# Kernel optimization log

Measured on AMD Instinct MI355X. Metric: run time of the kernel, lower is better.

## Reference

```python
import jax, jax.numpy as jnp
import numpy as np

N_NODES = 50000
N_EDGES = 800000
IN_C = 64
HID = 128
OUT_C = 2
N_GRAPHS = 64


def setup_inputs() -> dict:
    key = jax.random.key(0)
    ks = jax.random.split(key, 12)
    x = jax.random.normal(ks[0], (N_NODES, IN_C), dtype=jnp.float32)
    edge_index = jax.random.randint(ks[1], (2, N_EDGES), 0, N_NODES, dtype=jnp.int64)
    batch = jnp.sort(jax.random.randint(ks[2], (N_NODES,), 0, N_GRAPHS, dtype=jnp.int64))
    def glorot(k, shape):
        lim = float(np.sqrt(6.0 / (shape[0] + shape[1])))
        return jax.random.uniform(k, shape, dtype=jnp.float32, minval=-lim, maxval=lim)
    return {
        "x": x,
        "edge_index": edge_index,
        "batch": batch,
        "W1": glorot(ks[3], (IN_C, HID)),  "b1": jnp.zeros((HID,), jnp.float32),
        "W2": glorot(ks[4], (HID, HID)),   "b2": jnp.zeros((HID,), jnp.float32),
        "Wm1": glorot(ks[5], (HID, HID)),  "bm1": jnp.zeros((HID,), jnp.float32),
        "Wm2": glorot(ks[6], (HID, OUT_C)), "bm2": jnp.zeros((OUT_C,), jnp.float32),
    }


def reference(x, edge_index, batch, W1, b1, W2, b2, Wm1, bm1, Wm2, bm2):
    N = x.shape[0]
    # GCN normalization with self-loops (PyG GCNConv defaults)
    loops = jnp.arange(N, dtype=edge_index.dtype)
    src = jnp.concatenate([edge_index[0], loops])  # message sources
    dst = jnp.concatenate([edge_index[1], loops])  # aggregation targets
    deg = jax.ops.segment_sum(jnp.ones(dst.shape, x.dtype), dst, num_segments=N)
    dinv = jnp.where(deg > 0, jax.lax.rsqrt(deg), 0.0)
    norm = dinv[src] * dinv[dst]  # [E+N]

    def gcn_conv(h, W, b):
        h = h @ W                         # transform first (PyG order)
        msg = h[src] * norm[:, None]      # gather + normalize
        return jax.ops.segment_sum(msg, dst, num_segments=N) + b  # scatter-add

    h = jax.nn.relu(gcn_conv(x, W1, b1))
    # dropout is identity in eval mode
    h = gcn_conv(h, W2, b2)

    # global mean pool over graphs
    sums = jax.ops.segment_sum(h, batch, num_segments=N_GRAPHS)
    cnt = jax.ops.segment_sum(jnp.ones((N,), h.dtype), batch, num_segments=N_GRAPHS)
    g = sums / jnp.maximum(cnt, 1.0)[:, None]  # [G, HID]

    g = jax.nn.relu(g @ Wm1 + bm1)
    return g @ Wm2 + bm2  # [G, OUT_C]
```

## Files before the change

kernel.cpp:

```cpp
#include <hip/hip_runtime.h>
#include <stdint.h>

#define N_NODES 50000
#define N_EDGES 800000
#define IN_C 64
#define HID 128
#define OUT_C 2
#define N_GRAPHS 64
#define NBUCK 196
#define BCAP 6144
#define ECH 4096

typedef long long i64;
typedef __attribute__((ext_vector_type(8))) short bf8;
typedef __attribute__((ext_vector_type(4))) float f32x4;

__device__ __forceinline__ float bf2f(ushort h) {
    return __uint_as_float(((uint)h) << 16);
}
__device__ __forceinline__ ushort f2bf(float f) {
    uint x = __float_as_uint(f);
    uint r = x + 0x7fffu + ((x >> 16) & 1u);
    return (ushort)(r >> 16);
}
__device__ __forceinline__ float loadf(const void* p, size_t i, int bf) {
    return bf ? bf2f(((const ushort*)p)[i]) : ((const float*)p)[i];
}
__device__ __forceinline__ int clampi(int v, int lo, int hi) {
    return min(max(v, lo), hi);
}

__device__ __forceinline__ int edge_src(const void* ei, int e, int wide) {
    return wide ? (int)((const i64*)ei)[e] : ((const int*)ei)[e];
}
__device__ __forceinline__ int edge_dst(const void* ei, int e, int wide) {
    return wide ? (int)((const i64*)ei)[N_EDGES + e] : ((const int*)ei)[N_EDGES + e];
}
__device__ __forceinline__ i64 batch_at(const void* b, int i, int wide) {
    return wide ? ((const i64*)b)[i] : (i64)((const int*)b)[i];
}

__global__ __launch_bounds__(256) void k_init(const uint* __restrict__ braw,
                                              const uint* __restrict__ xraw,
                                              int* __restrict__ bcnt,
                                              float* __restrict__ gbuf,
                                              int* __restrict__ iflag,
                                              int* __restrict__ fflag) {
    int i = blockIdx.x * blockDim.x + threadIdx.x;
    if (i < N_GRAPHS * HID) gbuf[i] = 0.f;
    if (i < NBUCK) bcnt[i] = 0;
    if (blockIdx.x == 0) {
        __shared__ uint si[128];
        __shared__ int sf[256];
        int t = threadIdx.x;
        if (t < 128) si[t] = (t < 100) ? braw[25001 + 2 * t] : 0u;
        uint e = (xraw[t] >> 7) & 0xFFu;
        sf[t] = (e >= 100u && e <= 140u) ? 1 : 0;
        __syncthreads();
        for (int off = 128; off > 0; off >>= 1) {
            if (t < off) {
                sf[t] += sf[t + off];
                if (off <= 64 && t < 64) si[t] |= si[t + off];
            }
            __syncthreads();
        }
        if (t == 0) {
            *iflag = (si[0] == 0u) ? 1 : 0;
            *fflag = (sf[0] >= 192) ? 1 : 0;
        }
    }
}

__global__ __launch_bounds__(1024) void k_binA(const void* __restrict__ ei,
                                               const int* __restrict__ iflag,
                                               const int* __restrict__ fflag,
                                               const void* __restrict__ W1,
                                               const void* __restrict__ W2,
                                               ushort* __restrict__ Wt1,
                                               ushort* __restrict__ Wt2,
                                               int* __restrict__ bcnt,
                                               uint2* __restrict__ bmem) {
    int t = threadIdx.x;
    if (t < 256 && blockIdx.x < (IN_C * HID + HID * HID) / 256) {
        int ff = *fflag;
        int idx = blockIdx.x * 256 + t;
        if (idx < IN_C * HID) {
            int k = idx >> 7, n = idx & 127;
            Wt1[n * IN_C + k] = f2bf(loadf(W1, idx, ff));
        } else {
            int j = idx - IN_C * HID;
            int k = j >> 7, n = j & 127;
            Wt2[n * HID + k] = f2bf(loadf(W2, j, ff));
        }
    }
    int wide = *iflag;
    __shared__ int cnt[NBUCK];
    __shared__ int obase[NBUCK];
    __shared__ int run[NBUCK];
    __shared__ int gbase[NBUCK];
    __shared__ int sc[256];
    __shared__ uint2 stage[ECH];
    int e0 = blockIdx.x * ECH;
    int m = min(ECH, N_EDGES - e0);
    for (int i = t; i < NBUCK; i += 1024) cnt[i] = 0;
    __syncthreads();
    for (int i = t; i < m; i += 1024) {
        int d = edge_dst(ei, e0 + i, wide);
        atomicAdd(&cnt[d >> 8], 1);
    }
    __syncthreads();
    int cv = (t < NBUCK) ? cnt[t] : 0;
    if (t < 256) sc[t] = cv;
    __syncthreads();
    for (int off = 1; off < 256; off <<= 1) {
        int v = (t >= off && t < 256) ? sc[t - off] : 0;
        __syncthreads();
        if (t < 256) sc[t] += v;
        __syncthreads();
    }
    if (t < NBUCK) {
        int ex = sc[t] - cv;
        obase[t] = ex;
        run[t] = ex;
        gbase[t] = (cv > 0) ? atomicAdd(&bcnt[t], cv) : 0;
    }
    __syncthreads();
    for (int i = t; i < m; i += 1024) {
        int s = edge_src(ei, e0 + i, wide);
        int d = edge_dst(ei, e0 + i, wide);
        int slot = atomicAdd(&run[d >> 8], 1);
        uint2 pr;
        pr.x = (uint)s;
        pr.y = (uint)d;
        stage[slot] = pr;
    }
    __syncthreads();
    for (int i = t; i < m; i += 1024) {
        uint2 pr = stage[i];
        int b = (int)(pr.y >> 8);
        int pos = gbase[b] + (i - obase[b]);
        if (pos < BCAP) bmem[(size_t)b * BCAP + pos] = pr;
    }
}

__global__ __launch_bounds__(1024) void k_binB(const uint2* __restrict__ bmem,
                                               const int* __restrict__ bcnt,
                                               const void* __restrict__ x,
                                               const int* __restrict__ fflag,
                                               int* __restrict__ offs,
                                               int* __restrict__ csr,
                                               float* __restrict__ dinv,
                                               ushort* __restrict__ Y1) {
    int b = blockIdx.x;
    int t = threadIdx.x;
    int node0 = b << 8;
    __shared__ int sc[256];
    __shared__ int degl[256];
    __shared__ int run[256];
    __shared__ float sdinv[256];
    __shared__ int sbase, scnt;
    __shared__ int stage[BCAP];
    int v = (t < NBUCK) ? bcnt[t] : 0;
    if (t < 256) sc[t] = v;
    __syncthreads();
    for (int off = 1; off < 256; off <<= 1) {
        int u = (t >= off && t < 256) ? sc[t - off] : 0;
        __syncthreads();
        if (t < 256) sc[t] += u;
        __syncthreads();
    }
    if (t == b) {
        int c = clampi(v, 0, BCAP);
        scnt = c;
        sbase = clampi(sc[t] - v, 0, N_EDGES - c);
    }
    if (t < 256) degl[t] = 0;
    __syncthreads();
    int cnt = scnt;
    int base = sbase;
    for (int i = t; i < cnt; i += 1024) {
        uint2 pr = bmem[(size_t)b * BCAP + i];
        atomicAdd(&degl[pr.y & 255], 1);
    }
    __syncthreads();
    int dv = (t < 256) ? degl[t] : 0;
    if (t < 256) sc[t] = dv;
    __syncthreads();
    for (int off = 1; off < 256; off <<= 1) {
        int u = (t >= off && t < 256) ? sc[t - off] : 0;
        __syncthreads();
        if (t < 256) sc[t] += u;
        __syncthreads();
    }
    if (t < 256) {
        int ex = sc[t] - dv;
        run[t] = ex;
        float di = rsqrtf((float)(dv + 1));
        sdinv[t] = di;
        int n = node0 + t;
        if (n < N_NODES) {
            offs[n] = base + ex;
            dinv[n] = di;
        }
    }
    if (b == 0 && t == 0) offs[N_NODES] = N_EDGES;
    __syncthreads();
    for (int i = t; i < cnt; i += 1024) {
        uint2 pr = bmem[(size_t)b * BCAP + i];
        int slot = atomicAdd(&run[pr.y & 255], 1);
        stage[clampi(slot, 0, BCAP - 1)] = (int)pr.x;
    }
    __syncthreads();
    for (int i = t; i < cnt; i += 1024) csr[base + i] = stage[i];
    int ff = *fflag;
    for (int idx = t; idx < 256 * (IN_C / 4); idx += 1024) {
        int nl = idx >> 4, c4 = (idx & 15) * 4;
        int nn = node0 + nl;
        if (nn < N_NODES) {
            float x0, x1, x2, x3;
            if (ff) {
                const ushort* xp = (const ushort*)x + (size_t)nn * IN_C + c4;
                ushort4 u = *(const ushort4*)xp;
                x0 = bf2f(u.x); x1 = bf2f(u.y); x2 = bf2f(u.z); x3 = bf2f(u.w);
            } else {
                const float* xp = (const float*)x + (size_t)nn * IN_C + c4;
                float4 vv = *(const float4*)xp;
                x0 = vv.x; x1 = vv.y; x2 = vv.z; x3 = vv.w;
            }
            float di = sdinv[nl];
            ushort4 o;
            o.x = f2bf(x0 * di); o.y = f2bf(x1 * di);
            o.z = f2bf(x2 * di); o.w = f2bf(x3 * di);
            *(ushort4*)(Y1 + (size_t)nn * IN_C + c4) = o;
        }
    }
}

__global__ __launch_bounds__(256) void k_aggM(const ushort* __restrict__ Y1,
                                              const float* __restrict__ dinv,
                                              const int* __restrict__ offs,
                                              const int* __restrict__ csr,
                                              ushort* __restrict__ M) {
    int n = (blockIdx.x * blockDim.x + threadIdx.x) >> 4;
    int lane = threadIdx.x & 15;
    if (n >= N_NODES) return;
    const uint* y32 = (const uint*)Y1;
    size_t rb = (size_t)n * 32;
    uint s0 = y32[rb + lane];
    uint s1 = y32[rb + lane + 16];
    float a0 = bf2f((ushort)(s0 & 0xffffu));
    float a1 = bf2f((ushort)(s0 >> 16));
    float a2 = bf2f((ushort)(s1 & 0xffffu));
    float a3 = bf2f((ushort)(s1 >> 16));
    int s = offs[n];
    int e = min(offs[n + 1], s + 4096);
    int i = s;
    for (; i + 8 <= e; i += 8) {
        uint u0[8], u1[8];
#pragma unroll
        for (int k = 0; k < 8; k++) {
            size_t r = (size_t)csr[i + k] * 32;
            u0[k] = y32[r + lane];
            u1[k] = y32[r + lane + 16];
        }
#pragma unroll
        for (int k = 0; k < 8; k++) {
            a0 += bf2f((ushort)(u0[k] & 0xffffu));
            a1 += bf2f((ushort)(u0[k] >> 16));
            a2 += bf2f((ushort)(u1[k] & 0xffffu));
            a3 += bf2f((ushort)(u1[k] >> 16));
        }
    }
    for (; i < e; i++) {
        size_t r = (size_t)csr[i] * 32;
        uint u0 = y32[r + lane];
        uint u1 = y32[r + lane + 16];
        a0 += bf2f((ushort)(u0 & 0xffffu));
        a1 += bf2f((ushort)(u0 >> 16));
        a2 += bf2f((ushort)(u1 & 0xffffu));
        a3 += bf2f((ushort)(u1 >> 16));
    }
    float dv = dinv[n];
    ((uint*)M)[rb + lane] = ((uint)f2bf(a1 * dv) << 16) | (uint)f2bf(a0 * dv);
    ((uint*)M)[rb + lane + 16] = ((uint)f2bf(a3 * dv) << 16) | (uint)f2bf(a2 * dv);
}

__global__ __launch_bounds__(256) void k_agg128(const ushort* __restrict__ hs,
                                                const float* __restrict__ dinv,
                                                const int* __restrict__ offs,
                                                const int* __restrict__ csr,
                                                ushort* __restrict__ out) {
    int n = (blockIdx.x * blockDim.x + threadIdx.x) >> 5;
    int lane = threadIdx.x & 31;
    if (n >= N_NODES) return;
    const uint* hs32 = (const uint*)hs;
    size_t rb = (size_t)n * 64;
    uint s0 = hs32[rb + lane];
    uint s1 = hs32[rb + lane + 32];
    float a0 = bf2f((ushort)(s0 & 0xffffu));
    float a1 = bf2f((ushort)(s0 >> 16));
    float a2 = bf2f((ushort)(s1 & 0xffffu));
    float a3 = bf2f((ushort)(s1 >> 16));
    int s = offs[n];
    int e = min(offs[n + 1], s + 4096);
    int i = s;
    for (; i + 8 <= e; i += 8) {
        uint u0[8], u1[8];
#pragma unroll
        for (int k = 0; k < 8; k++) {
            size_t r = (size_t)csr[i + k] * 64;
            u0[k] = hs32[r + lane];
            u1[k] = hs32[r + lane + 32];
        }
#pragma unroll
        for (int k = 0; k < 8; k++) {
            a0 += bf2f((ushort)(u0[k] & 0xffffu));
            a1 += bf2f((ushort)(u0[k] >> 16));
            a2 += bf2f((ushort)(u1[k] & 0xffffu));
            a3 += bf2f((ushort)(u1[k] >> 16));
        }
    }
    for (; i < e; i++) {
        size_t r = (size_t)csr[i] * 64;
        uint u0 = hs32[r + lane];
        uint u1 = hs32[r + lane + 32];
        a0 += bf2f((ushort)(u0 & 0xffffu));
        a1 += bf2f((ushort)(u0 >> 16));
        a2 += bf2f((ushort)(u1 & 0xffffu));
        a3 += bf2f((ushort)(u1 >> 16));
    }
    float dv = dinv[n];
    ((uint*)out)[rb + lane] = ((uint)f2bf(a1 * dv) << 16) | (uint)f2bf(a0 * dv);
    ((uint*)out)[rb + lane + 32] = ((uint)f2bf(a3 * dv) << 16) | (uint)f2bf(a2 * dv);
}

template <int K>
__global__ __launch_bounds__(256) void k_gemm_f(const ushort* __restrict__ A,
                                                const ushort* __restrict__ Wt,
                                                const int* __restrict__ fflag,
                                                const float* __restrict__ dinv,
                                                const void* __restrict__ bias,
                                                ushort* __restrict__ out) {
    int ff = *fflag;
    int wave = threadIdx.x >> 6;
    int lane = threadIdx.x & 63;
    int m16 = lane & 15;
    int q = lane >> 4;
    int rowbase = blockIdx.x * 64 + wave * 16;
    int arow = min(rowbase + m16, N_NODES - 1);

    f32x4 acc[8];
#pragma unroll
    for (int t = 0; t < 8; t++) acc[t] = (f32x4){0.f, 0.f, 0.f, 0.f};

#pragma unroll
    for (int kc = 0; kc < K; kc += 32) {
        bf8 a = *(const bf8*)(A + (size_t)arow * K + kc + q * 8);
#pragma unroll
        for (int t = 0; t < 8; t++) {
            bf8 b = *(const bf8*)(Wt + (size_t)(t * 16 + m16) * K + kc + q * 8);
            acc[t] = __builtin_amdgcn_mfma_f32_16x16x32_bf16(a, b, acc[t], 0, 0, 0);
        }
    }

    float dv[4];
    int rowok[4];
#pragma unroll
    for (int r = 0; r < 4; r++) {
        int row = rowbase + q * 4 + r;
        rowok[r] = (row < N_NODES);
        dv[r] = rowok[r] ? dinv[row] : 1.f;
    }
#pragma unroll
    for (int t = 0; t < 8; t++) {
        int col = t * 16 + m16;
        float bv = loadf(bias, col, ff);
#pragma unroll
        for (int r = 0; r < 4; r++) {
            int row = rowbase + q * 4 + r;
            if (rowok[r]) {
                float v = fmaxf(acc[t][r] + bv, 0.f) * dv[r];
                out[(size_t)row * HID + col] = f2bf(v);
            }
        }
    }
}

__global__ __launch_bounds__(256) void k_gemm_pool(const ushort* __restrict__ A,
                                                   const ushort* __restrict__ Wt,
                                                   const void* __restrict__ batch,
                                                   const int* __restrict__ iflag,
                                                   float* __restrict__ gsum) {
    const int K = HID;
    int wide = *iflag;
    int tid = threadIdx.x;
    int wave = tid >> 6;
    int lane = tid & 63;
    int m16 = lane & 15;
    int q = lane >> 4;
    int rowbase = blockIdx.x * 64 + wave * 16;
    int arow = min(rowbase + m16, N_NODES - 1);

    __shared__ float sacc[64][HID];
    __shared__ int sbg[64];

    if (tid < 64) {
        int n = blockIdx.x * 64 + tid;
        int g = (n < N_NODES) ? (int)batch_at(batch, n, wide) : -1;
        sbg[tid] = (g < 0 || g >= N_GRAPHS) ? -1 : g;
    }

    f32x4 acc[8];
#pragma unroll
    for (int t = 0; t < 8; t++) acc[t] = (f32x4){0.f, 0.f, 0.f, 0.f};

#pragma unroll
    for (int kc = 0; kc < K; kc += 32) {
        bf8 a = *(const bf8*)(A + (size_t)arow * K + kc + q * 8);
#pragma unroll
        for (int t = 0; t < 8; t++) {
            bf8 b = *(const bf8*)(Wt + (size_t)(t * 16 + m16) * K + kc + q * 8);
            acc[t] = __builtin_amdgcn_mfma_f32_16x16x32_bf16(a, b, acc[t], 0, 0, 0);
        }
    }

#pragma unroll
    for (int t = 0; t < 8; t++) {
        int col = t * 16 + m16;
#pragma unroll
        for (int r = 0; r < 4; r++) {
            int rl = wave * 16 + q * 4 + r;
            int row = rowbase + q * 4 + r;
            sacc[rl][col] = (row < N_NODES) ? acc[t][r] : 0.f;
        }
    }
    __syncthreads();

    int col = tid & 127;
    int half = tid >> 7;
    int gcur = -1;
    float a = 0.f;
    for (int r = half * 32; r < half * 32 + 32; r++) {
        int g = sbg[r];
        if (g != gcur) {
            if (gcur >= 0) atomicAdd(&gsum[gcur * HID + col], a);
            a = 0.f;
            gcur = g;
        }
        a += sacc[r][col];
    }
    if (gcur >= 0) atomicAdd(&gsum[gcur * HID + col], a);
}

__global__ void k_mlp(const float* __restrict__ gsum, const void* __restrict__ batch,
                      const int* __restrict__ iflag, const void* __restrict__ b2,
                      const void* __restrict__ Wm1, const void* __restrict__ bm1,
                      const void* __restrict__ Wm2, const void* __restrict__ bm2,
                      const int* __restrict__ fflag, float* __restrict__ out) {
    int ff = *fflag;
    int wide = *iflag;
    int gr = blockIdx.x;
    int c = threadIdx.x;
    int lo = 0, hi = N_NODES;
    while (lo < hi) { int m = (lo + hi) >> 1; if (batch_at(batch, m, wide) < (i64)gr) lo = m + 1; else hi = m; }
    int s = lo;
    lo = s; hi = N_NODES;
    while (lo < hi) { int m = (lo + hi) >> 1; if (batch_at(batch, m, wide) < (i64)(gr + 1)) lo = m + 1; else hi = m; }
    float cnt = (float)(lo - s);

    __shared__ float sg[HID];
    __shared__ float r0[HID], r1[HID];
    sg[c] = gsum[gr * HID + c] / fmaxf(cnt, 1.0f) + loadf(b2, c, ff);
    __syncthreads();
    float acc = loadf(bm1, c, ff);
#pragma unroll 8
    for (int k = 0; k < HID; k++) acc += sg[k] * loadf(Wm1, k * HID + c, ff);
    float hid = fmaxf(acc, 0.f);
    r0[c] = hid * loadf(Wm2, c * OUT_C + 0, ff);
    r1[c] = hid * loadf(Wm2, c * OUT_C + 1, ff);
    __syncthreads();
    for (int off = 64; off > 0; off >>= 1) {
        if (c < off) { r0[c] += r0[c + off]; r1[c] += r1[c + off]; }
        __syncthreads();
    }
    if (c == 0) {
        out[gr * OUT_C + 0] = r0[0] + loadf(bm2, 0, ff);
        out[gr * OUT_C + 1] = r1[0] + loadf(bm2, 1, ff);
    }
}


extern "C" void kernel_launch(void* const* d_in, const int* in_sizes, int n_in,
                              void* d_out, int out_size, void* d_ws, size_t ws_size,
                              hipStream_t stream) {
    const void* x     = d_in[0];
    const void* ei    = d_in[1];
    const void* batch = d_in[2];
    const void* W1  = d_in[3];
    const void* b1  = d_in[4];
    const void* W2  = d_in[5];
    const void* b2  = d_in[6];
    const void* Wm1 = d_in[7];
    const void* bm1 = d_in[8];
    const void* Wm2 = d_in[9];
    const void* bm2 = d_in[10];

    char* p = (char*)d_ws;
    auto alloc = [&](size_t bytes) {
        char* r = p;
        p += (bytes + 255) & ~(size_t)255;
        return r;
    };
    int*    iflag  = (int*)alloc(4);
    int*    fflag  = (int*)alloc(4);
    int*    bcnt   = (int*)alloc(NBUCK * 4);
    uint2*  bmem   = (uint2*)alloc((size_t)NBUCK * BCAP * 8);
    float*  dinv   = (float*)alloc(N_NODES * 4);
    int*    offs   = (int*)alloc((N_NODES + 1) * 4);
    int*    csr    = (int*)alloc(N_EDGES * 4);
    ushort* Wt1    = (ushort*)alloc(IN_C * HID * 2);
    ushort* Wt2    = (ushort*)alloc(HID * HID * 2);
    ushort* Y1     = (ushort*)alloc((size_t)N_NODES * IN_C * 2);
    ushort* Mbuf   = (ushort*)alloc((size_t)N_NODES * IN_C * 2);
    ushort* h1s    = (ushort*)alloc((size_t)N_NODES * HID * 2);
    ushort* N2     = (ushort*)alloc((size_t)N_NODES * HID * 2);
    float*  gbuf   = (float*)alloc(N_GRAPHS * HID * 4);

    k_init<<<(N_GRAPHS * HID + 255) / 256, 256, 0, stream>>>(
        (const uint*)batch, (const uint*)x, bcnt, gbuf, iflag, fflag);
    k_binA<<<(N_EDGES + ECH - 1) / ECH, 1024, 0, stream>>>(
        ei, iflag, fflag, W1, W2, Wt1, Wt2, bcnt, bmem);
    k_binB<<<NBUCK, 1024, 0, stream>>>(bmem, bcnt, x, fflag, offs, csr, dinv, Y1);

    k_aggM<<<(N_NODES * 16 + 255) / 256, 256, 0, stream>>>(Y1, dinv, offs, csr, Mbuf);
    k_gemm_f<IN_C><<<(N_NODES + 63) / 64, 256, 0, stream>>>(Mbuf, Wt1, fflag, dinv, b1, h1s);
    k_agg128<<<(N_NODES * 32 + 255) / 256, 256, 0, stream>>>(h1s, dinv, offs, csr, N2);
    k_gemm_pool<<<(N_NODES + 63) / 64, 256, 0, stream>>>(N2, Wt2, batch, iflag, gbuf);

    k_mlp<<<N_GRAPHS, HID, 0, stream>>>(gbuf, batch, iflag, b2, Wm1, bm1, Wm2, bm2, fflag, (float*)d_out);
}
```

Baseline: 204.2 us.

## Fuse all pipeline stages into one persistent kernel with grid barriers

Replaces the sequence of binning, aggregation, GEMM, pooling and MLP kernels with one persistent 256-block kernel. The stages are separated by atomic-counter grid barriers, and each stage runs as a grid-stride loop over the same blocks. This removes launch overhead and inter-kernel gaps, but it depends on all 256 blocks of 1024 threads being co-resident. The shared-memory union and the split-K MFMA with shared atomics in the pool stage may also lower occupancy and per-stage efficiency, and the spin barrier has a timeout fallback that could break correctness.

```diff
diff --git a/kernel.cpp b/kernel.cpp
--- a/kernel.cpp
+++ b/kernel.cpp
@@ -9,7 +9,11 @@
 #define N_GRAPHS 64
 #define NBUCK 196
 #define BCAP 6144
-#define ECH 4096
+#define MECH 3125
+#define MCHUNK 256
+#define NTILE 782
+#define GRID 256
+#define TPB 1024
 
 typedef long long i64;
 typedef __attribute__((ext_vector_type(8))) short bf8;
@@ -40,15 +44,33 @@
     return wide ? ((const i64*)b)[i] : (i64)((const int*)b)[i];
 }
 
-__global__ __launch_bounds__(256) void k_init(const uint* __restrict__ braw,
+__device__ __forceinline__ void gbar(int* __restrict__ bars, int idx) {
+    __syncthreads();
+    if (threadIdx.x == 0) {
+        __threadfence();
+        __hip_atomic_fetch_add(&bars[idx], 1, __ATOMIC_ACQ_REL,
+                               __HIP_MEMORY_SCOPE_AGENT);
+        long long spin = 0;
+        while (__hip_atomic_load(&bars[idx], __ATOMIC_ACQUIRE,
+                                 __HIP_MEMORY_SCOPE_AGENT) < GRID) {
+            __builtin_amdgcn_s_sleep(8);
+            if (++spin > 2000000) break;
+        }
+    }
+    __syncthreads();
+}
+
+__global__ __launch_bounds__(256) void k_prep(const uint* __restrict__ braw,
                                               const uint* __restrict__ xraw,
+                                              int* __restrict__ bars,
                                               int* __restrict__ bcnt,
                                               float* __restrict__ gbuf,
                                               int* __restrict__ iflag,
                                               int* __restrict__ fflag) {
     int i = blockIdx.x * blockDim.x + threadIdx.x;
+    if (i < 16) bars[i] = 0;
+    if (i < NBUCK) bcnt[i] = 0;
     if (i < N_GRAPHS * HID) gbuf[i] = 0.f;
-    if (i < NBUCK) bcnt[i] = 0;
     if (blockIdx.x == 0) {
         __shared__ uint si[128];
         __shared__ int sf[256];
@@ -71,421 +93,414 @@
     }
 }
 
-__global__ __launch_bounds__(1024) void k_binA(const void* __restrict__ ei,
-                                               const int* __restrict__ iflag,
-                                               const int* __restrict__ fflag,
-                                               const void* __restrict__ W1,
-                                               const void* __restrict__ W2,
-                                               ushort* __restrict__ Wt1,
-                                               ushort* __restrict__ Wt2,
-                                               int* __restrict__ bcnt,
-                                               uint2* __restrict__ bmem) {
-    int t = threadIdx.x;
-    if (t < 256 && blockIdx.x < (IN_C * HID + HID * HID) / 256) {
+
+struct SmA {
+    int cnt[NBUCK]; int obase[NBUCK]; int run[NBUCK]; int gbase[NBUCK];
+    int sc[256]; uint2 stage[MECH];
+};
+struct SmB {
+    int sc[256]; int degl[256]; int run[256]; float sdinv[256];
+    int sbase, scnt; int stage[BCAP];
+};
+struct SmP {
+    float sacc[64][HID]; int sbg[64];
+};
+struct SmM {
+    float sg[8][HID]; float r0[8][HID]; float r1[8][HID];
+};
+union MegaSm { SmA a; SmB b; SmP p; SmM m; };
+
+__global__ __launch_bounds__(TPB) void k_mega(
+    const void* __restrict__ x, const void* __restrict__ ei,
+    const void* __restrict__ batch,
+    const void* __restrict__ W1, const void* __restrict__ b1,
+    const void* __restrict__ W2, const void* __restrict__ b2,
+    const void* __restrict__ Wm1, const void* __restrict__ bm1,
+    const void* __restrict__ Wm2, const void* __restrict__ bm2,
+    int* __restrict__ bars, int* __restrict__ bcnt, uint2* __restrict__ bmem,
+    float* __restrict__ dinv, int* __restrict__ offs, int* __restrict__ csr,
+    ushort* __restrict__ Wt1, ushort* __restrict__ Wt2,
+    ushort* __restrict__ Y1, ushort* __restrict__ Mbuf,
+    ushort* __restrict__ h1s, ushort* __restrict__ N2,
+    float* __restrict__ gbuf, const int* __restrict__ iflag,
+    const int* __restrict__ fflag, float* __restrict__ outp) {
+    __shared__ MegaSm sm;
+    int tid = threadIdx.x;
+    int gsz = gridDim.x;
+
+    {
         int ff = *fflag;
-        int idx = blockIdx.x * 256 + t;
-        if (idx < IN_C * HID) {
-            int k = idx >> 7, n = idx & 127;
-            Wt1[n * IN_C + k] = f2bf(loadf(W1, idx, ff));
-        } else {
-            int j = idx - IN_C * HID;
-            int k = j >> 7, n = j & 127;
-            Wt2[n * HID + k] = f2bf(loadf(W2, j, ff));
-        }
-    }
-    int wide = *iflag;
-    __shared__ int cnt[NBUCK];
-    __shared__ int obase[NBUCK];
-    __shared__ int run[NBUCK];
-    __shared__ int gbase[NBUCK];
-    __shared__ int sc[256];
-    __shared__ uint2 stage[ECH];
-    int e0 = blockIdx.x * ECH;
-    int m = min(ECH, N_EDGES - e0);
-    for (int i = t; i < NBUCK; i += 1024) cnt[i] = 0;
-    __syncthreads();
-    for (int i = t; i < m; i += 1024) {
-        int d = edge_dst(ei, e0 + i, wide);
-        atomicAdd(&cnt[d >> 8], 1);
-    }
-    __syncthreads();
-    int cv = (t < NBUCK) ? cnt[t] : 0;
-    if (t < 256) sc[t] = cv;
-    __syncthreads();
-    for (int off = 1; off < 256; off <<= 1) {
-        int v = (t >= off && t < 256) ? sc[t - off] : 0;
-        __syncthreads();
-        if (t < 256) sc[t] += v;
-        __syncthreads();
-    }
-    if (t < NBUCK) {
-        int ex = sc[t] - cv;
-        obase[t] = ex;
-        run[t] = ex;
-        gbase[t] = (cv > 0) ? atomicAdd(&bcnt[t], cv) : 0;
-    }
-    __syncthreads();
-    for (int i = t; i < m; i += 1024) {
-        int s = edge_src(ei, e0 + i, wide);
-        int d = edge_dst(ei, e0 + i, wide);
-        int slot = atomicAdd(&run[d >> 8], 1);
-        uint2 pr;
-        pr.x = (uint)s;
-        pr.y = (uint)d;
-        stage[slot] = pr;
-    }
-    __syncthreads();
-    for (int i = t; i < m; i += 1024) {
-        uint2 pr = stage[i];
-        int b = (int)(pr.y >> 8);
-        int pos = gbase[b] + (i - obase[b]);
-        if (pos < BCAP) bmem[(size_t)b * BCAP + pos] = pr;
-    }
-}
-
-__global__ __launch_bounds__(1024) void k_binB(const uint2* __restrict__ bmem,
-                                               const int* __restrict__ bcnt,
-                                               const void* __restrict__ x,
-                                               const int* __restrict__ fflag,
-                                               int* __restrict__ offs,
-                                               int* __restrict__ csr,
-                                               float* __restrict__ dinv,
-                                               ushort* __restrict__ Y1) {
-    int b = blockIdx.x;
-    int t = threadIdx.x;
-    int node0 = b << 8;
-    __shared__ int sc[256];
-    __shared__ int degl[256];
-    __shared__ int run[256];
-    __shared__ float sdinv[256];
-    __shared__ int sbase, scnt;
-    __shared__ int stage[BCAP];
-    int v = (t < NBUCK) ? bcnt[t] : 0;
-    if (t < 256) sc[t] = v;
-    __syncthreads();
-    for (int off = 1; off < 256; off <<= 1) {
-        int u = (t >= off && t < 256) ? sc[t - off] : 0;
-        __syncthreads();
-        if (t < 256) sc[t] += u;
-        __syncthreads();
-    }
-    if (t == b) {
-        int c = clampi(v, 0, BCAP);
-        scnt = c;
-        sbase = clampi(sc[t] - v, 0, N_EDGES - c);
-    }
-    if (t < 256) degl[t] = 0;
-    __syncthreads();
-    int cnt = scnt;
-    int base = sbase;
-    for (int i = t; i < cnt; i += 1024) {
-        uint2 pr = bmem[(size_t)b * BCAP + i];
-        atomicAdd(&degl[pr.y & 255], 1);
-    }
-    __syncthreads();
-    int dv = (t < 256) ? degl[t] : 0;
-    if (t < 256) sc[t] = dv;
-    __syncthreads();
-    for (int off = 1; off < 256; off <<= 1) {
-        int u = (t >= off && t < 256) ? sc[t - off] : 0;
-        __syncthreads();
-        if (t < 256) sc[t] += u;
-        __syncthreads();
-    }
-    if (t < 256) {
-        int ex = sc[t] - dv;
-        run[t] = ex;
-        float di = rsqrtf((float)(dv + 1));
-        sdinv[t] = di;
-        int n = node0 + t;
-        if (n < N_NODES) {
-            offs[n] = base + ex;
-            dinv[n] = di;
-        }
-    }
-    if (b == 0 && t == 0) offs[N_NODES] = N_EDGES;
-    __syncthreads();
-    for (int i = t; i < cnt; i += 1024) {
-        uint2 pr = bmem[(size_t)b * BCAP + i];
-        int slot = atomicAdd(&run[pr.y & 255], 1);
-        stage[clampi(slot, 0, BCAP - 1)] = (int)pr.x;
-    }
-    __syncthreads();
-    for (int i = t; i < cnt; i += 1024) csr[base + i] = stage[i];
-    int ff = *fflag;
-    for (int idx = t; idx < 256 * (IN_C / 4); idx += 1024) {
-        int nl = idx >> 4, c4 = (idx & 15) * 4;
-        int nn = node0 + nl;
-        if (nn < N_NODES) {
-            float x0, x1, x2, x3;
-            if (ff) {
-                const ushort* xp = (const ushort*)x + (size_t)nn * IN_C + c4;
-                ushort4 u = *(const ushort4*)xp;
-                x0 = bf2f(u.x); x1 = bf2f(u.y); x2 = bf2f(u.z); x3 = bf2f(u.w);
-            } else {
-                const float* xp = (const float*)x + (size_t)nn * IN_C + c4;
-                float4 vv = *(const float4*)xp;
-                x0 = vv.x; x1 = vv.y; x2 = vv.z; x3 = vv.w;
-            }
-            float di = sdinv[nl];
-            ushort4 o;
-            o.x = f2bf(x0 * di); o.y = f2bf(x1 * di);
-            o.z = f2bf(x2 * di); o.w = f2bf(x3 * di);
-            *(ushort4*)(Y1 + (size_t)nn * IN_C + c4) = o;
-        }
-    }
-}
-
-__global__ __launch_bounds__(256) void k_aggM(const ushort* __restrict__ Y1,
-                                              const float* __restrict__ dinv,
-                                              const int* __restrict__ offs,
-                                              const int* __restrict__ csr,
-                                              ushort* __restrict__ M) {
-    int n = (blockIdx.x * blockDim.x + threadIdx.x) >> 4;
-    int lane = threadIdx.x & 15;
-    if (n >= N_NODES) return;
-    const uint* y32 = (const uint*)Y1;
-    size_t rb = (size_t)n * 32;
-    uint s0 = y32[rb + lane];
-    uint s1 = y32[rb + lane + 16];
-    float a0 = bf2f((ushort)(s0 & 0xffffu));
-    float a1 = bf2f((ushort)(s0 >> 16));
-    float a2 = bf2f((ushort)(s1 & 0xffffu));
-    float a3 = bf2f((ushort)(s1 >> 16));
-    int s = offs[n];
-    int e = min(offs[n + 1], s + 4096);
-    int i = s;
-    for (; i + 8 <= e; i += 8) {
-        uint u0[8], u1[8];
-#pragma unroll
-        for (int k = 0; k < 8; k++) {
-            size_t r = (size_t)csr[i + k] * 32;
-            u0[k] = y32[r + lane];
-            u1[k] = y32[r + lane + 16];
-        }
-#pragma unroll
-        for (int k = 0; k < 8; k++) {
-            a0 += bf2f((ushort)(u0[k] & 0xffffu));
-            a1 += bf2f((ushort)(u0[k] >> 16));
-            a2 += bf2f((ushort)(u1[k] & 0xffffu));
-            a3 += bf2f((ushort)(u1[k] >> 16));
-        }
-    }
-    for (; i < e; i++) {
-        size_t r = (size_t)csr[i] * 32;
-        uint u0 = y32[r + lane];
-        uint u1 = y32[r + lane + 16];
-        a0 += bf2f((ushort)(u0 & 0xffffu));
-        a1 += bf2f((ushort)(u0 >> 16));
-        a2 += bf2f((ushort)(u1 & 0xffffu));
-        a3 += bf2f((ushort)(u1 >> 16));
-    }
-    float dv = dinv[n];
-    ((uint*)M)[rb + lane] = ((uint)f2bf(a1 * dv) << 16) | (uint)f2bf(a0 * dv);
-    ((uint*)M)[rb + lane + 16] = ((uint)f2bf(a3 * dv) << 16) | (uint)f2bf(a2 * dv);
-}
-
-__global__ __launch_bounds__(256) void k_agg128(const ushort* __restrict__ hs,
-                                                const float* __restrict__ dinv,
-                                                const int* __restrict__ offs,
-                                                const int* __restrict__ csr,
-                                                ushort* __restrict__ out) {
-    int n = (blockIdx.x * blockDim.x + threadIdx.x) >> 5;
-    int lane = threadIdx.x & 31;
-    if (n >= N_NODES) return;
-    const uint* hs32 = (const uint*)hs;
-    size_t rb = (size_t)n * 64;
-    uint s0 = hs32[rb + lane];
-    uint s1 = hs32[rb + lane + 32];
-    float a0 = bf2f((ushort)(s0 & 0xffffu));
-    float a1 = bf2f((ushort)(s0 >> 16));
-    float a2 = bf2f((ushort)(s1 & 0xffffu));
-    float a3 = bf2f((ushort)(s1 >> 16));
-    int s = offs[n];
-    int e = min(offs[n + 1], s + 4096);
-    int i = s;
-    for (; i + 8 <= e; i += 8) {
-        uint u0[8], u1[8];
-#pragma unroll
-        for (int k = 0; k < 8; k++) {
-            size_t r = (size_t)csr[i + k] * 64;
-            u0[k] = hs32[r + lane];
-            u1[k] = hs32[r + lane + 32];
-        }
-#pragma unroll
-        for (int k = 0; k < 8; k++) {
-            a0 += bf2f((ushort)(u0[k] & 0xffffu));
-            a1 += bf2f((ushort)(u0[k] >> 16));
-            a2 += bf2f((ushort)(u1[k] & 0xffffu));
-            a3 += bf2f((ushort)(u1[k] >> 16));
-        }
-    }
-    for (; i < e; i++) {
-        size_t r = (size_t)csr[i] * 64;
-        uint u0 = hs32[r + lane];
-        uint u1 = hs32[r + lane + 32];
-        a0 += bf2f((ushort)(u0 & 0xffffu));
-        a1 += bf2f((ushort)(u0 >> 16));
-        a2 += bf2f((ushort)(u1 & 0xffffu));
-        a3 += bf2f((ushort)(u1 >> 16));
-    }
-    float dv = dinv[n];
-    ((uint*)out)[rb + lane] = ((uint)f2bf(a1 * dv) << 16) | (uint)f2bf(a0 * dv);
-    ((uint*)out)[rb + lane + 32] = ((uint)f2bf(a3 * dv) << 16) | (uint)f2bf(a2 * dv);
-}
-
-template <int K>
-__global__ __launch_bounds__(256) void k_gemm_f(const ushort* __restrict__ A,
-                                                const ushort* __restrict__ Wt,
-                                                const int* __restrict__ fflag,
-                                                const float* __restrict__ dinv,
-                                                const void* __restrict__ bias,
-                                                ushort* __restrict__ out) {
-    int ff = *fflag;
-    int wave = threadIdx.x >> 6;
-    int lane = threadIdx.x & 63;
-    int m16 = lane & 15;
-    int q = lane >> 4;
-    int rowbase = blockIdx.x * 64 + wave * 16;
-    int arow = min(rowbase + m16, N_NODES - 1);
-
-    f32x4 acc[8];
-#pragma unroll
-    for (int t = 0; t < 8; t++) acc[t] = (f32x4){0.f, 0.f, 0.f, 0.f};
-
-#pragma unroll
-    for (int kc = 0; kc < K; kc += 32) {
-        bf8 a = *(const bf8*)(A + (size_t)arow * K + kc + q * 8);
-#pragma unroll
-        for (int t = 0; t < 8; t++) {
-            bf8 b = *(const bf8*)(Wt + (size_t)(t * 16 + m16) * K + kc + q * 8);
-            acc[t] = __builtin_amdgcn_mfma_f32_16x16x32_bf16(a, b, acc[t], 0, 0, 0);
-        }
-    }
-
-    float dv[4];
-    int rowok[4];
-#pragma unroll
-    for (int r = 0; r < 4; r++) {
-        int row = rowbase + q * 4 + r;
-        rowok[r] = (row < N_NODES);
-        dv[r] = rowok[r] ? dinv[row] : 1.f;
-    }
-#pragma unroll
-    for (int t = 0; t < 8; t++) {
-        int col = t * 16 + m16;
-        float bv = loadf(bias, col, ff);
-#pragma unroll
-        for (int r = 0; r < 4; r++) {
-            int row = rowbase + q * 4 + r;
-            if (rowok[r]) {
-                float v = fmaxf(acc[t][r] + bv, 0.f) * dv[r];
-                out[(size_t)row * HID + col] = f2bf(v);
-            }
-        }
-    }
-}
-
-__global__ __launch_bounds__(256) void k_gemm_pool(const ushort* __restrict__ A,
-                                                   const ushort* __restrict__ Wt,
-                                                   const void* __restrict__ batch,
-                                                   const int* __restrict__ iflag,
-                                                   float* __restrict__ gsum) {
-    const int K = HID;
-    int wide = *iflag;
-    int tid = threadIdx.x;
-    int wave = tid >> 6;
-    int lane = tid & 63;
-    int m16 = lane & 15;
-    int q = lane >> 4;
-    int rowbase = blockIdx.x * 64 + wave * 16;
-    int arow = min(rowbase + m16, N_NODES - 1);
-
-    __shared__ float sacc[64][HID];
-    __shared__ int sbg[64];
-
-    if (tid < 64) {
-        int n = blockIdx.x * 64 + tid;
-        int g = (n < N_NODES) ? (int)batch_at(batch, n, wide) : -1;
-        sbg[tid] = (g < 0 || g >= N_GRAPHS) ? -1 : g;
-    }
-
-    f32x4 acc[8];
-#pragma unroll
-    for (int t = 0; t < 8; t++) acc[t] = (f32x4){0.f, 0.f, 0.f, 0.f};
-
-#pragma unroll
-    for (int kc = 0; kc < K; kc += 32) {
-        bf8 a = *(const bf8*)(A + (size_t)arow * K + kc + q * 8);
-#pragma unroll
-        for (int t = 0; t < 8; t++) {
-            bf8 b = *(const bf8*)(Wt + (size_t)(t * 16 + m16) * K + kc + q * 8);
-            acc[t] = __builtin_amdgcn_mfma_f32_16x16x32_bf16(a, b, acc[t], 0, 0, 0);
-        }
-    }
-
-#pragma unroll
-    for (int t = 0; t < 8; t++) {
-        int col = t * 16 + m16;
-#pragma unroll
-        for (int r = 0; r < 4; r++) {
-            int rl = wave * 16 + q * 4 + r;
-            int row = rowbase + q * 4 + r;
-            sacc[rl][col] = (row < N_NODES) ? acc[t][r] : 0.f;
-        }
-    }
-    __syncthreads();
-
-    int col = tid & 127;
-    int half = tid >> 7;
-    int gcur = -1;
-    float a = 0.f;
-    for (int r = half * 32; r < half * 32 + 32; r++) {
-        int g = sbg[r];
-        if (g != gcur) {
-            if (gcur >= 0) atomicAdd(&gsum[gcur * HID + col], a);
-            a = 0.f;
-            gcur = g;
-        }
-        a += sacc[r][col];
-    }
-    if (gcur >= 0) atomicAdd(&gsum[gcur * HID + col], a);
-}
-
-__global__ void k_mlp(const float* __restrict__ gsum, const void* __restrict__ batch,
-                      const int* __restrict__ iflag, const void* __restrict__ b2,
-                      const void* __restrict__ Wm1, const void* __restrict__ bm1,
-                      const void* __restrict__ Wm2, const void* __restrict__ bm2,
-                      const int* __restrict__ fflag, float* __restrict__ out) {
-    int ff = *fflag;
-    int wide = *iflag;
-    int gr = blockIdx.x;
-    int c = threadIdx.x;
-    int lo = 0, hi = N_NODES;
-    while (lo < hi) { int m = (lo + hi) >> 1; if (batch_at(batch, m, wide) < (i64)gr) lo = m + 1; else hi = m; }
-    int s = lo;
-    lo = s; hi = N_NODES;
-    while (lo < hi) { int m = (lo + hi) >> 1; if (batch_at(batch, m, wide) < (i64)(gr + 1)) lo = m + 1; else hi = m; }
-    float cnt = (float)(lo - s);
-
-    __shared__ float sg[HID];
-    __shared__ float r0[HID], r1[HID];
-    sg[c] = gsum[gr * HID + c] / fmaxf(cnt, 1.0f) + loadf(b2, c, ff);
-    __syncthreads();
-    float acc = loadf(bm1, c, ff);
+        for (int w = blockIdx.x; w < 24; w += gsz) {
+            int idx = w * 1024 + tid;
+            if (idx < IN_C * HID) {
+                int k = idx >> 7, n = idx & 127;
+                Wt1[n * IN_C + k] = f2bf(loadf(W1, idx, ff));
+            } else if (idx < IN_C * HID + HID * HID) {
+                int j = idx - IN_C * HID;
+                int k = j >> 7, n = j & 127;
+                Wt2[n * HID + k] = f2bf(loadf(W2, j, ff));
+            }
+        }
+        int wide = *iflag;
+        for (int ch = blockIdx.x; ch < MCHUNK; ch += gsz) {
+            int e0 = ch * MECH;
+            __syncthreads();
+            for (int i = tid; i < NBUCK; i += TPB) sm.a.cnt[i] = 0;
+            __syncthreads();
+            for (int i = tid; i < MECH; i += TPB) {
+                int d = edge_dst(ei, e0 + i, wide);
+                atomicAdd(&sm.a.cnt[d >> 8], 1);
+            }
+            __syncthreads();
+            int cv = (tid < NBUCK) ? sm.a.cnt[tid] : 0;
+            if (tid < 256) sm.a.sc[tid] = cv;
+            __syncthreads();
+            for (int off = 1; off < 256; off <<= 1) {
+                int v = (tid >= off && tid < 256) ? sm.a.sc[tid - off] : 0;
+                __syncthreads();
+                if (tid < 256) sm.a.sc[tid] += v;
+                __syncthreads();
+            }
+            if (tid < NBUCK) {
+                int ex = sm.a.sc[tid] - cv;
+                sm.a.obase[tid] = ex;
+                sm.a.run[tid] = ex;
+                sm.a.gbase[tid] = (cv > 0) ? atomicAdd(&bcnt[tid], cv) : 0;
+            }
+            __syncthreads();
+            for (int i = tid; i < MECH; i += TPB) {
+                int s = edge_src(ei, e0 + i, wide);
+                int d = edge_dst(ei, e0 + i, wide);
+                int slot = atomicAdd(&sm.a.run[d >> 8], 1);
+                uint2 pr; pr.x = (uint)s; pr.y = (uint)d;
+                sm.a.stage[slot] = pr;
+            }
+            __syncthreads();
+            for (int i = tid; i < MECH; i += TPB) {
+                uint2 pr = sm.a.stage[i];
+                int b = (int)(pr.y >> 8);
+                int pos = sm.a.gbase[b] + (i - sm.a.obase[b]);
+                if (pos < BCAP) bmem[(size_t)b * BCAP + pos] = pr;
+            }
+        }
+    }
+    gbar(bars, 0);
+
+    {
+        int ff = *fflag;
+        for (int bk = blockIdx.x; bk < NBUCK; bk += gsz) {
+            int node0 = bk << 8;
+            __syncthreads();
+            int v = (tid < NBUCK) ? bcnt[tid] : 0;
+            if (tid < 256) sm.b.sc[tid] = v;
+            __syncthreads();
+            for (int off = 1; off < 256; off <<= 1) {
+                int u = (tid >= off && tid < 256) ? sm.b.sc[tid - off] : 0;
+                __syncthreads();
+                if (tid < 256) sm.b.sc[tid] += u;
+                __syncthreads();
+            }
+            if (tid == bk) {
+                int c = clampi(v, 0, BCAP);
+                sm.b.scnt = c;
+                sm.b.sbase = clampi(sm.b.sc[tid] - v, 0, N_EDGES - c);
+            }
+            if (tid < 256) sm.b.degl[tid] = 0;
+            __syncthreads();
+            int cnt = sm.b.scnt;
+            int base = sm.b.sbase;
+            for (int i = tid; i < cnt; i += TPB) {
+                uint2 pr = bmem[(size_t)bk * BCAP + i];
+                atomicAdd(&sm.b.degl[pr.y & 255], 1);
+            }
+            __syncthreads();
+            int dv = (tid < 256) ? sm.b.degl[tid] : 0;
+            if (tid < 256) sm.b.sc[tid] = dv;
+            __syncthreads();
+            for (int off = 1; off < 256; off <<= 1) {
+                int u = (tid >= off && tid < 256) ? sm.b.sc[tid - off] : 0;
+                __syncthreads();
+                if (tid < 256) sm.b.sc[tid] += u;
+                __syncthreads();
+            }
+            if (tid < 256) {
+                int ex = sm.b.sc[tid] - dv;
+                sm.b.run[tid] = ex;
+                float di = rsqrtf((float)(dv + 1));
+                sm.b.sdinv[tid] = di;
+                int n = node0 + tid;
+                if (n < N_NODES) { offs[n] = base + ex; dinv[n] = di; }
+            }
+            if (bk == 0 && tid == 0) offs[N_NODES] = N_EDGES;
+            __syncthreads();
+            for (int i = tid; i < cnt; i += TPB) {
+                uint2 pr = bmem[(size_t)bk * BCAP + i];
+                int slot = atomicAdd(&sm.b.run[pr.y & 255], 1);
+                sm.b.stage[clampi(slot, 0, BCAP - 1)] = (int)pr.x;
+            }
+            __syncthreads();
+            for (int i = tid; i < cnt; i += TPB) csr[base + i] = sm.b.stage[i];
+            for (int idx = tid; idx < 256 * (IN_C / 4); idx += TPB) {
+                int nl = idx >> 4, c4 = (idx & 15) * 4;
+                int nn = node0 + nl;
+                if (nn < N_NODES) {
+                    float x0, x1, x2, x3;
+                    if (ff) {
+                        ushort4 u = *(const ushort4*)((const ushort*)x + (size_t)nn * IN_C + c4);
+                        x0 = bf2f(u.x); x1 = bf2f(u.y); x2 = bf2f(u.z); x3 = bf2f(u.w);
+                    } else {
+                        float4 vv = *(const float4*)((const float*)x + (size_t)nn * IN_C + c4);
+                        x0 = vv.x; x1 = vv.y; x2 = vv.z; x3 = vv.w;
+                    }
+                    float di = sm.b.sdinv[nl];
+                    ushort4 o;
+                    o.x = f2bf(x0 * di); o.y = f2bf(x1 * di);
+                    o.z = f2bf(x2 * di); o.w = f2bf(x3 * di);
+                    *(ushort4*)(Y1 + (size_t)nn * IN_C + c4) = o;
+                }
+            }
+        }
+    }
+    gbar(bars, 1);
+
+    {
+        int g = blockIdx.x * TPB + tid;
+        int lane = g & 15;
+        int step = (gsz * TPB) >> 4;
+        const uint* y32 = (const uint*)Y1;
+        for (int n = g >> 4; n < N_NODES; n += step) {
+            size_t rb = (size_t)n * 32;
+            uint s0 = y32[rb + lane];
+            uint s1 = y32[rb + lane + 16];
+            float a0 = bf2f((ushort)(s0 & 0xffffu));
+            float a1 = bf2f((ushort)(s0 >> 16));
+            float a2 = bf2f((ushort)(s1 & 0xffffu));
+            float a3 = bf2f((ushort)(s1 >> 16));
+            int s = offs[n];
+            int e = min(offs[n + 1], s + 4096);
+            int i = s;
+            for (; i + 8 <= e; i += 8) {
+                uint u0[8], u1[8];
+#pragma unroll
+                for (int k = 0; k < 8; k++) {
+                    size_t r = (size_t)csr[i + k] * 32;
+                    u0[k] = y32[r + lane];
+                    u1[k] = y32[r + lane + 16];
+                }
+#pragma unroll
+                for (int k = 0; k < 8; k++) {
+                    a0 += bf2f((ushort)(u0[k] & 0xffffu));
+                    a1 += bf2f((ushort)(u0[k] >> 16));
+                    a2 += bf2f((ushort)(u1[k] & 0xffffu));
+                    a3 += bf2f((ushort)(u1[k] >> 16));
+                }
+            }
+            for (; i < e; i++) {
+                size_t r = (size_t)csr[i] * 32;
+                uint u0 = y32[r + lane];
+                uint u1 = y32[r + lane + 16];
+                a0 += bf2f((ushort)(u0 & 0xffffu));
+                a1 += bf2f((ushort)(u0 >> 16));
+                a2 += bf2f((ushort)(u1 & 0xffffu));
+                a3 += bf2f((ushort)(u1 >> 16));
+            }
+            float dvv = dinv[n];
+            ((uint*)Mbuf)[rb + lane] = ((uint)f2bf(a1 * dvv) << 16) | (uint)f2bf(a0 * dvv);
+            ((uint*)Mbuf)[rb + lane + 16] = ((uint)f2bf(a3 * dvv) << 16) | (uint)f2bf(a2 * dvv);
+        }
+    }
+    gbar(bars, 2);
+
+    {
+        int ff = *fflag;
+        int group = tid >> 8;
+        int subwave = (tid & 255) >> 6;
+        int lane = tid & 63;
+        int m16 = lane & 15, q = lane >> 4;
+        for (int tb = blockIdx.x * 4 + group; tb < NTILE; tb += gsz * 4) {
+            int rowbase = tb * 64 + subwave * 16;
+            int arow = min(rowbase + m16, N_NODES - 1);
+            f32x4 acc[8];
+#pragma unroll
+            for (int t = 0; t < 8; t++) acc[t] = (f32x4){0.f, 0.f, 0.f, 0.f};
+#pragma unroll
+            for (int kc = 0; kc < IN_C; kc += 32) {
+                bf8 a = *(const bf8*)(Mbuf + (size_t)arow * IN_C + kc + q * 8);
+#pragma unroll
+                for (int t = 0; t < 8; t++) {
+                    bf8 b = *(const bf8*)(Wt1 + (size_t)(t * 16 + m16) * IN_C + kc + q * 8);
+                    acc[t] = __builtin_amdgcn_mfma_f32_16x16x32_bf16(a, b, acc[t], 0, 0, 0);
+                }
+            }
+            float dvr[4];
+            int rowok[4];
+#pragma unroll
+            for (int r = 0; r < 4; r++) {
+                int row = rowbase + q * 4 + r;
+                rowok[r] = (row < N_NODES);
+                dvr[r] = rowok[r] ? dinv[row] : 1.f;
+            }
+#pragma unroll
+            for (int t = 0; t < 8; t++) {
+                int col = t * 16 + m16;
+                float bv = loadf(b1, col, ff);
+#pragma unroll
+                for (int r = 0; r < 4; r++) {
+                    int row = rowbase + q * 4 + r;
+                    if (rowok[r]) {
+                        float v = fmaxf(acc[t][r] + bv, 0.f) * dvr[r];
+                        h1s[(size_t)row * HID + col] = f2bf(v);
+                    }
+                }
+            }
+        }
+    }
+    gbar(bars, 3);
+
+    {
+        int g = blockIdx.x * TPB + tid;
+        int lane = g & 31;
+        int step = (gsz * TPB) >> 5;
+        const uint* hs32 = (const uint*)h1s;
+        for (int n = g >> 5; n < N_NODES; n += step) {
+            size_t rb = (size_t)n * 64;
+            uint s0 = hs32[rb + lane];
+            uint s1 = hs32[rb + lane + 32];
+            float a0 = bf2f((ushort)(s0 & 0xffffu));
+            float a1 = bf2f((ushort)(s0 >> 16));
+            float a2 = bf2f((ushort)(s1 & 0xffffu));
+            float a3 = bf2f((ushort)(s1 >> 16));
+            int s = offs[n];
+            int e = min(offs[n + 1], s + 4096);
+            int i = s;
+            for (; i + 8 <= e; i += 8) {
+                uint u0[8], u1[8];
+#pragma unroll
+                for (int k = 0; k < 8; k++) {
+                    size_t r = (size_t)csr[i + k] * 64;
+                    u0[k] = hs32[r + lane];
+                    u1[k] = hs32[r + lane + 32];
+                }
+#pragma unroll
+                for (int k = 0; k < 8; k++) {
+                    a0 += bf2f((ushort)(u0[k] & 0xffffu));
+                    a1 += bf2f((ushort)(u0[k] >> 16));
+                    a2 += bf2f((ushort)(u1[k] & 0xffffu));
+                    a3 += bf2f((ushort)(u1[k] >> 16));
+                }
+            }
+            for (; i < e; i++) {
+                size_t r = (size_t)csr[i] * 64;
+                uint u0 = hs32[r + lane];
+                uint u1 = hs32[r + lane + 32];
+                a0 += bf2f((ushort)(u0 & 0xffffu));
+                a1 += bf2f((ushort)(u0 >> 16));
+                a2 += bf2f((ushort)(u1 & 0xffffu));
+                a3 += bf2f((ushort)(u1 >> 16));
+            }
+            float dvv = dinv[n];
+            ((uint*)N2)[rb + lane] = ((uint)f2bf(a1 * dvv) << 16) | (uint)f2bf(a0 * dvv);
+            ((uint*)N2)[rb + lane + 32] = ((uint)f2bf(a3 * dvv) << 16) | (uint)f2bf(a2 * dvv);
+        }
+    }
+    gbar(bars, 4);
+
+    {
+        int wide = *iflag;
+        int wave = tid >> 6;
+        int strip = wave & 3;
+        int ksl = wave >> 2;
+        int lane = tid & 63;
+        int m16 = lane & 15, q = lane >> 4;
+        for (int tile = blockIdx.x; tile < NTILE; tile += gsz) {
+            for (int i = tid; i < 64 * HID; i += TPB) ((float*)sm.p.sacc)[i] = 0.f;
+            if (tid < 64) {
+                int n = tile * 64 + tid;
+                int g = (n < N_NODES) ? (int)batch_at(batch, n, wide) : -1;
+                sm.p.sbg[tid] = (g < 0 || g >= N_GRAPHS) ? -1 : g;
+            }
+            __syncthreads();
+            int rowbase = tile * 64 + strip * 16;
+            int arow = min(rowbase + m16, N_NODES - 1);
+            int kc = ksl * 32;
+            f32x4 acc[8];
+#pragma unroll
+            for (int t = 0; t < 8; t++) acc[t] = (f32x4){0.f, 0.f, 0.f, 0.f};
+            bf8 a = *(const bf8*)(N2 + (size_t)arow * HID + kc + q * 8);
+#pragma unroll
+            for (int t = 0; t < 8; t++) {
+                bf8 b = *(const bf8*)(Wt2 + (size_t)(t * 16 + m16) * HID + kc + q * 8);
+                acc[t] = __builtin_amdgcn_mfma_f32_16x16x32_bf16(a, b, acc[t], 0, 0, 0);
+            }
+#pragma unroll
+            for (int t = 0; t < 8; t++) {
+                int col = t * 16 + m16;
+#pragma unroll
+                for (int r = 0; r < 4; r++) {
+                    int rl = strip * 16 + q * 4 + r;
+                    int row = rowbase + q * 4 + r;
+                    if (row < N_NODES) atomicAdd(&sm.p.sacc[rl][col], acc[t][r]);
+                }
+            }
+            __syncthreads();
+            int col = tid & 127;
+            int rc = tid >> 7;
+            int gcur = -1;
+            float aa = 0.f;
+            for (int r = rc * 8; r < rc * 8 + 8; r++) {
+                int g = sm.p.sbg[r];
+                if (g != gcur) {
+                    if (gcur >= 0) atomicAdd(&gbuf[gcur * HID + col], aa);
+                    aa = 0.f;
+                    gcur = g;
+                }
+                aa += sm.p.sacc[r][col];
+            }
+            if (gcur >= 0) atomicAdd(&gbuf[gcur * HID + col], aa);
+            __syncthreads();
+        }
+    }
+    gbar(bars, 5);
+
+    {
+        int ff = *fflag;
+        int wide = *iflag;
+        int group = tid >> 7;
+        int c = tid & 127;
+        int gr = blockIdx.x * 8 + group;
+        bool act = (gr < N_GRAPHS);
+        if (blockIdx.x * 8 < N_GRAPHS) {
+            if (act) {
+                int lo = 0, hi = N_NODES;
+                while (lo < hi) { int m = (lo + hi) >> 1; if (batch_at(batch, m, wide) < (i64)gr) lo = m + 1; else hi = m; }
+                int s = lo;
+                lo = s; hi = N_NODES;
+                while (lo < hi) { int m = (lo + hi) >> 1; if (batch_at(batch, m, wide) < (i64)(gr + 1)) lo = m + 1; else hi = m; }
+                float cntf = fmaxf((float)(lo - s), 1.0f);
+                sm.m.sg[group][c] = gbuf[gr * HID + c] / cntf + loadf(b2, c, ff);
+            }
+            __syncthreads();
+            if (act) {
+                float acc = loadf(bm1, c, ff);
 #pragma unroll 8
-    for (int k = 0; k < HID; k++) acc += sg[k] * loadf(Wm1, k * HID + c, ff);
-    float hid = fmaxf(acc, 0.f);
-    r0[c] = hid * loadf(Wm2, c * OUT_C + 0, ff);
-    r1[c] = hid * loadf(Wm2, c * OUT_C + 1, ff);
-    __syncthreads();
-    for (int off = 64; off > 0; off >>= 1) {
-        if (c < off) { r0[c] += r0[c + off]; r1[c] += r1[c + off]; }
-        __syncthreads();
-    }
-    if (c == 0) {
-        out[gr * OUT_C + 0] = r0[0] + loadf(bm2, 0, ff);
-        out[gr * OUT_C + 1] = r1[0] + loadf(bm2, 1, ff);
+                for (int k = 0; k < HID; k++) acc += sm.m.sg[group][k] * loadf(Wm1, k * HID + c, ff);
+                float hid = fmaxf(acc, 0.f);
+                sm.m.r0[group][c] = hid * loadf(Wm2, c * OUT_C + 0, ff);
+                sm.m.r1[group][c] = hid * loadf(Wm2, c * OUT_C + 1, ff);
+            }
+            __syncthreads();
+            for (int off = 64; off > 0; off >>= 1) {
+                if (act && c < off) {
+                    sm.m.r0[group][c] += sm.m.r0[group][c + off];
+                    sm.m.r1[group][c] += sm.m.r1[group][c + off];
+                }
+                __syncthreads();
+            }
+            if (act && c == 0) {
+                outp[gr * OUT_C + 0] = sm.m.r0[group][0] + loadf(bm2, 0, ff);
+                outp[gr * OUT_C + 1] = sm.m.r1[group][0] + loadf(bm2, 1, ff);
+            }
+        }
     }
 }
 
@@ -511,6 +526,7 @@
         p += (bytes + 255) & ~(size_t)255;
         return r;
     };
+    int*    bars   = (int*)alloc(16 * 4);
     int*    iflag  = (int*)alloc(4);
     int*    fflag  = (int*)alloc(4);
     int*    bcnt   = (int*)alloc(NBUCK * 4);
@@ -525,17 +541,12 @@
     ushort* h1s    = (ushort*)alloc((size_t)N_NODES * HID * 2);
     ushort* N2     = (ushort*)alloc((size_t)N_NODES * HID * 2);
     float*  gbuf   = (float*)alloc(N_GRAPHS * HID * 4);
-
-    k_init<<<(N_GRAPHS * HID + 255) / 256, 256, 0, stream>>>(
-        (const uint*)batch, (const uint*)x, bcnt, gbuf, iflag, fflag);
-    k_binA<<<(N_EDGES + ECH - 1) / ECH, 1024, 0, stream>>>(
-        ei, iflag, fflag, W1, W2, Wt1, Wt2, bcnt, bmem);
-    k_binB<<<NBUCK, 1024, 0, stream>>>(bmem, bcnt, x, fflag, offs, csr, dinv, Y1);
-
-    k_aggM<<<(N_NODES * 16 + 255) / 256, 256, 0, stream>>>(Y1, dinv, offs, csr, Mbuf);
-    k_gemm_f<IN_C><<<(N_NODES + 63) / 64, 256, 0, stream>>>(Mbuf, Wt1, fflag, dinv, b1, h1s);
-    k_agg128<<<(N_NODES * 32 + 255) / 256, 256, 0, stream>>>(h1s, dinv, offs, csr, N2);
-    k_gemm_pool<<<(N_NODES + 63) / 64, 256, 0, stream>>>(N2, Wt2, batch, iflag, gbuf);
-
-    k_mlp<<<N_GRAPHS, HID, 0, stream>>>(gbuf, batch, iflag, b2, Wm1, bm1, Wm2, bm2, fflag, (float*)d_out);
-}
+    float*  outp   = (float*)d_out;
+
+    k_prep<<<(N_GRAPHS * HID + 255) / 256, 256, 0, stream>>>(
+        (const uint*)batch, (const uint*)x, bars, bcnt, gbuf, iflag, fflag);
+    k_mega<<<GRID, TPB, 0, stream>>>(
+        x, ei, batch, W1, b1, W2, b2, Wm1, bm1, Wm2, bm2,
+        bars, bcnt, bmem, dinv, offs, csr, Wt1, Wt2, Y1, Mbuf,
+        h1s, N2, gbuf, iflag, fflag, outp);
+}
```

After: 599.1 us. +193.4%, slower.
